# Performance work log

Hardware: AMD Instinct MI355X
Metric: run time of the kernel (lower is better)

Reference implementation:

```python
import jax, jax.numpy as jnp
import numpy as np

B, T, H, W, C = 2, 16, 56, 56, 128
K_T, K = 5, 7
HIDDEN = 4 * C  # expansion_ratio = 4


def kernel_to_freq_3d(kernel, t, h, w):
    # kernel: (C, k_t, k_h, k_w) -> (C, t, h, w) complex freq, centered circular placement
    c, k_t, k_h, k_w = kernel.shape
    t_idx = (jnp.arange(k_t) - k_t // 2) % t
    h_idx = (jnp.arange(k_h) - k_h // 2) % h
    w_idx = (jnp.arange(k_w) - k_w // 2) % w
    tt, th, tw = jnp.meshgrid(t_idx, h_idx, w_idx, indexing='ij')
    padded = jnp.zeros((c, t, h, w), kernel.dtype).at[:, tt, th, tw].set(kernel)
    return jnp.fft.fftn(padded, axes=(1, 2, 3))


def setup_inputs() -> dict:
    key = jax.random.key(0)
    ks = jax.random.split(key, 16)
    n = lambda k, shape, s=0.02: (jax.random.normal(k, shape, jnp.float32) * s)
    return {
        'x': jax.random.normal(ks[0], (B, T, H, W, C), jnp.float32),
        'Wg': n(ks[1], (C, C)), 'bg': jnp.zeros((C,), jnp.float32),
        'Wh': n(ks[2], (C, C)), 'bh': jnp.zeros((C,), jnp.float32),
        'gate_kernel': n(ks[3], (C, K_T, K, K), 0.05),
        'hidden_kernel': n(ks[4], (C, K_T, K, K), 0.05),
        'Wo': n(ks[5], (C, C)), 'bo': jnp.zeros((C,), jnp.float32),
        'ln_scale': jnp.ones((C,), jnp.float32), 'ln_bias': jnp.zeros((C,), jnp.float32),
        'W1': n(ks[6], (C, HIDDEN)), 'b1': jnp.zeros((HIDDEN,), jnp.float32),
        'W2': n(ks[7], (HIDDEN, C)), 'b2': jnp.zeros((C,), jnp.float32),
        'gamma': jnp.full((C,), 1e-6, jnp.float32),
    }


def reference(x, Wg, bg, Wh, bh, gate_kernel, hidden_kernel, Wo, bo,
              ln_scale, ln_bias, W1, b1, W2, b2, gamma):
    b, t, h, w, c = x.shape
    residual = x
    # --- GatedConvSSM3D ---
    gate_proj = x @ Wg + bg
    hidden_proj = x @ Wh + bh
    gk_f = kernel_to_freq_3d(gate_kernel, t, h, w).transpose(1, 2, 3, 0)   # (T,H,W,C)
    hk_f = kernel_to_freq_3d(hidden_kernel, t, h, w).transpose(1, 2, 3, 0)
    gate_spatial = jnp.fft.ifftn(jnp.fft.fftn(gate_proj, axes=(1, 2, 3)) * gk_f[None], axes=(1, 2, 3)).real
    hidden_spatial = jnp.fft.ifftn(jnp.fft.fftn(hidden_proj, axes=(1, 2, 3)) * hk_f[None], axes=(1, 2, 3)).real
    log_forget = -jax.nn.softplus(gate_spatial)          # log(1 - z)
    log_values = -jax.nn.softplus(-gate_spatial) + jnp.log(hidden_spatial ** 2 + 1e-6)  # log z + log h~

    def op(left, right):
        la, lb = left
        ra, rb = right
        return (la + ra, jnp.logaddexp(ra + lb, rb))

    # Heinsen scan along temporal axis (axis=1 of (B,T,H,W,C))
    _, log_h = jax.lax.associative_scan(op, (log_forget, log_values), axis=1)
    ssm_out = jnp.exp(log_h) @ Wo + bo
    # --- LayerNorm3D ---
    mean = jnp.mean(ssm_out, axis=-1, keepdims=True)
    var = jnp.var(ssm_out, axis=-1, keepdims=True)
    xn = (ssm_out - mean) / jnp.sqrt(var + 1e-6) * ln_scale + ln_bias
    # --- MLP + LayerScale + residual ---
    y = jax.nn.gelu(xn @ W1 + b1) @ W2 + b2
    return y * gamma + residual
```

## Files before the change

kernel.cpp:

```cpp
#include <hip/hip_runtime.h>
#include <hip/hip_bf16.h>
#include <hip/hip_fp16.h>
#include <cstdint>
#include <cstddef>

typedef unsigned short u16;
typedef __attribute__((ext_vector_type(8))) short bf16x8;
typedef __attribute__((ext_vector_type(4))) float f32x4;

#define MFMA16(a,b,c) __builtin_amdgcn_mfma_f32_16x16x32_bf16((a),(b),(c),0,0,0)


static __device__ __forceinline__ float b2f(u16 u){ return __uint_as_float(((unsigned)u)<<16); }
static __device__ __forceinline__ u16 f2b(float f){
  unsigned u = __float_as_uint(f);
  return (u16)((u + 0x7fffu + ((u>>16)&1u)) >> 16);
}
static __device__ __forceinline__ u16 f2h(float f){ return __half_as_ushort(__float2half(f)); }
static __device__ __forceinline__ __half2 u2h(unsigned u){ union{unsigned u;__half2 h;}c; c.u=u; return c.h; }

static __device__ __forceinline__ void gld_lds16(const void* g, void* l){
  __builtin_amdgcn_global_load_lds(
      (const __attribute__((address_space(1))) void*)g,
      (__attribute__((address_space(3))) void*)l, 16, 0, 0);
}

static __device__ __forceinline__ bool input_is_f32(const void* xp){
  const u16* u = (const u16*)xp;
  int cnt = 0;
#pragma unroll
  for (int i = 0; i < 64; ++i){
    unsigned e = (u[2*i] >> 7) & 0xFF;
    cnt += (e >= 100 && e <= 140) ? 1 : 0;
  }
  return cnt < 32;
}

static __device__ __forceinline__ u16 ldb(const void* p, int i, bool f32){
  return f32 ? f2b(((const float*)p)[i]) : ((const u16*)p)[i];
}
static __device__ __forceinline__ float ldf(const void* p, int i, bool f32){
  return f32 ? ((const float*)p)[i] : b2f(((const u16*)p)[i]);
}

__global__ __launch_bounds__(256) void k0_prep(
    const void* __restrict__ x,
    const void* __restrict__ Wg, const void* __restrict__ Wh, const void* __restrict__ Wo,
    const void* __restrict__ W1, const void* __restrict__ W2,
    const void* __restrict__ gk, const void* __restrict__ hk,
    const void* __restrict__ bg, const void* __restrict__ bh, const void* __restrict__ bo,
    const void* __restrict__ lns, const void* __restrict__ lnb,
    const void* __restrict__ b1, const void* __restrict__ b2, const void* __restrict__ gm,
    u16* __restrict__ XB,
    u16* __restrict__ WgT, u16* __restrict__ WhT, u16* __restrict__ WoT,
    u16* __restrict__ W1T, u16* __restrict__ W2T,
    unsigned* __restrict__ KWG, unsigned* __restrict__ KWH, u16* __restrict__ PRM)
{
  const bool f32 = input_is_f32(x);
  int tid = blockIdx.x*blockDim.x + threadIdx.x;
  int np  = gridDim.x*blockDim.x;

  if (f32){
    const float* xf = (const float*)x;
    for (int p = tid; p < 6422528; p += np){
      unsigned v = (unsigned)f2b(xf[2*p]) | ((unsigned)f2b(xf[2*p+1]) << 16);
      ((unsigned*)XB)[p] = v;
    }
  } else {
    const unsigned* xu = (const unsigned*)x;
    for (int p = tid; p < 6422528; p += np) ((unsigned*)XB)[p] = xu[p];
  }

  for (int p = tid; p < 16384; p += np){
    int n = p>>7, k = p&127;
    WgT[p] = ldb(Wg, k*128+n, f32);
    WhT[p] = ldb(Wh, k*128+n, f32);
    WoT[p] = ldb(Wo, k*128+n, f32);
  }
  for (int p = tid; p < 65536; p += np){
    int n = p>>7, k = p&127;
    W1T[p] = ldb(W1, k*512+n, f32);
  }
  for (int p = tid; p < 65536; p += np){
    int n = p>>9, k = p&511;
    W2T[p] = ldb(W2, k*128+n, f32);
  }
  for (int p = tid; p < 50176; p += np){
    int tap = p&7, c = (p>>3)&127, jk = p>>10;
    unsigned vg = 0, vh = 0;
    if (tap < 5){
      int s = (c*5+tap)*49 + jk;
      unsigned g16 = f2h(ldf(gk, s, f32)), h16 = f2h(ldf(hk, s, f32));
      vg = g16 | (g16<<16); vh = h16 | (h16<<16);
    }
    KWG[p] = vg; KWH[p] = vh;
  }
  for (int p = tid; p < 1408; p += np){
    const void* src; int off;
    if      (p < 128)  { src = bg;  off = p; }
    else if (p < 256)  { src = bh;  off = p-128; }
    else if (p < 384)  { src = bo;  off = p-256; }
    else if (p < 512)  { src = lns; off = p-384; }
    else if (p < 640)  { src = lnb; off = p-512; }
    else if (p < 1152) { src = b1;  off = p-640; }
    else if (p < 1280) { src = b2;  off = p-1152; }
    else               { src = gm;  off = p-1280; }
    PRM[p] = ldb(src, off, f32);
  }
}

__global__ __launch_bounds__(256) void k1_dualgemm(
    const u16* __restrict__ XB, const u16* __restrict__ WgT, const u16* __restrict__ WhT,
    const u16* __restrict__ PRM,
    u16* __restrict__ GP, u16* __restrict__ HP)
{
  int bid = blockIdx.x;
  int b = bid / 784; int hw = (bid % 784)*4 + (threadIdx.x >> 6);
  int lane = threadIdx.x & 63;
  int lrow = lane & 15, q = lane >> 4;

  bf16x8 a[4];
  const u16* xr = XB + ((size_t)(b*16 + lrow)*3136 + hw)*128 + q*8;
#pragma unroll
  for (int kt = 0; kt < 4; ++kt) a[kt] = *(const bf16x8*)(xr + kt*32);

#pragma unroll
  for (int mat = 0; mat < 2; ++mat){
    const u16* WT  = mat ? WhT : WgT;
    const u16* bia = PRM + (mat ? 128 : 0);
    u16* out       = mat ? HP  : GP;
#pragma unroll
    for (int nt = 0; nt < 8; ++nt){
      f32x4 acc = {0.f,0.f,0.f,0.f};
      const u16* wr = WT + (nt*16 + lrow)*128 + q*8;
#pragma unroll
      for (int kt = 0; kt < 4; ++kt){
        bf16x8 bfr = *(const bf16x8*)(wr + kt*32);
        acc = MFMA16(a[kt], bfr, acc);
      }
      int c = nt*16 + lrow;
      float bv = b2f(bia[c]);
      size_t base = (((size_t)(b*32 + (c>>2))*3136 + hw)*4 + (c&3))*16 + q*4;
      ushort4 pk;
      pk.x = f2h(acc[0] + bv); pk.y = f2h(acc[1] + bv);
      pk.z = f2h(acc[2] + bv); pk.w = f2h(acc[3] + bv);
      *(ushort4*)(out + base) = pk;
    }
  }
}

__global__ __launch_bounds__(256, 5) void k2_conv_scan(
    const u16* __restrict__ GP, const u16* __restrict__ HP,
    const unsigned* __restrict__ KWG, const unsigned* __restrict__ KWH,
    u16* __restrict__ ELH)
{
  __shared__ __align__(16) unsigned su[6272];
  __shared__ __align__(16) unsigned ku[1568];

  int bid = blockIdx.x;
  int b = bid / 1568; int rr = bid - b*1568;
  int cg = rr / 49; int s = rr % 49;
  int th = s / 7, tw = s % 7;
  int tid = threadIdx.x;
  int h0g = th*8, w0g = tw*8;
  size_t tb = (size_t)(b*32 + cg)*200704;

  int cl = tid & 3, w0 = (tid>>2)&7, h0 = tid>>5;
  int wv = tid >> 6, lane = tid & 63;

  unsigned soff[4]; bool sval[4];
#pragma unroll
  for (int ss = 0; ss < 4; ++ss){
    int idx = wv*64 + ss*256 + lane;
    sval[ss] = (idx < 784);
    int pos = idx >> 2, pcl = idx & 3;
    int hh = pos / 14, ww = pos - hh*14;
    int hg = h0g + hh - 3; if (hg < 0) hg += 56; else if (hg >= 56) hg -= 56;
    int wg = w0g + ww - 3; if (wg < 0) wg += 56; else if (wg >= 56) wg -= 56;
    soff[ss] = (unsigned)(((hg*56 + wg)*4 + pcl)*32);
  }
  const char* gpb = (const char*)(GP + tb);
  const char* hpb = (const char*)(HP + tb);

  auto wload = [&](const unsigned* KW){
    for (int p = tid; p < 1568; p += 256){
      int tap = p & 7, c2 = (p>>3)&3, jk = p>>5;
      ku[p] = KW[(jk*128 + cg*4 + c2)*8 + tap];
    }
  };
  auto stagepass = [&](const char* Pb){
#pragma unroll
    for (int half = 0; half < 2; ++half){
#pragma unroll
      for (int ss = 0; ss < 4; ++ss){
        if (sval[ss])
          gld_lds16(Pb + soff[ss] + half*16,
                    (char*)su + half*12544 + (wv*64 + ss*256)*16);
      }
    }
  };
  auto convpass = [&](__half2* A){
#pragma unroll
    for (int p = 0; p < 8; ++p) A[p] = u2h(0u);
    for (int j = 0; j < 7; ++j){
      int hh = h0 + 6 - j;
      int cb0 = ((hh*14 + w0)*4 + cl)*4;
      int wb0 = (j*28 + cl)*8;
#pragma unroll
      for (int k = 0; k < 7; ++k){
        const unsigned* sp = &su[cb0 + (6-k)*16];
        uint4 da = *(const uint4*)sp;
        uint4 db = *(const uint4*)(sp + 3136);
        unsigned P[8] = {da.x,da.y,da.z,da.w,db.x,db.y,db.z,db.w};
        unsigned M[8];
#pragma unroll
        for (int p = 0; p < 8; ++p) M[p] = (P[p]>>16) | (P[(p+1)&7]<<16);
        const unsigned* kp = &ku[wb0 + k*32];
        uint4 w4 = *(const uint4*)kp;
        unsigned w5 = kp[4];
#pragma unroll
        for (int p = 0; p < 8; ++p){
          A[p] = __hfma2(u2h(w4.x), u2h(P[(p+1)&7]), A[p]);
          A[p] = __hfma2(u2h(w4.y), u2h(M[p]),       A[p]);
          A[p] = __hfma2(u2h(w4.z), u2h(P[p]),       A[p]);
          A[p] = __hfma2(u2h(w4.w), u2h(M[(p+7)&7]), A[p]);
          A[p] = __hfma2(u2h(w5),   u2h(P[(p+7)&7]), A[p]);
        }
      }
    }
  };

  __half2 Ag[8], Ah[8];
  wload(KWG);
  stagepass(gpb);
  __syncthreads();
  convpass(Ag);
  __syncthreads();
  wload(KWH);
  stagepass(hpb);
  __syncthreads();
  convpass(Ah);

  float xg[16], xh[16];
#pragma unroll
  for (int p = 0; p < 8; ++p){
    float2 g2 = __half22float2(Ag[p]); xg[2*p] = g2.x; xg[2*p+1] = g2.y;
    float2 h2 = __half22float2(Ah[p]); xh[2*p] = h2.x; xh[2*p+1] = h2.y;
  }

  size_t ob = tb + ((size_t)(h0g + h0)*56 + (w0g + w0))*4 + cl;
  float lh = 0.f;
#pragma unroll
  for (int t = 0; t < 16; ++t){
    float g  = xg[t];
    float spg = fmaxf(g, 0.f) + __logf(1.f + __expf(-fabsf(g)));
    float lf  = -spg;
    float hv  = xh[t];
    float lv  = (g - spg) + __logf(hv*hv + 1e-6f);
    if (t == 0) lh = lv;
    else {
      float a_ = lf + lh;
      float mx = fmaxf(a_, lv);
      lh = mx + __logf(1.f + __expf(-fabsf(a_ - lv)));
    }
    ELH[ob + (size_t)t*12544] = f2b(__expf(lh));
  }
}

__global__ __launch_bounds__(256, 2) void k34_gemm_ln_mlp(
    const u16* __restrict__ ELH, const u16* __restrict__ WoT,
    const u16* __restrict__ W1T, const u16* __restrict__ W2T,
    const u16* __restrict__ PRM,
    const void* __restrict__ xraw, void* __restrict__ outv)
{
  __shared__ __align__(16) u16 smem[37376];
  u16* sW0 = smem;
  u16* sW1 = smem + 16384;
  u16* sXp = smem;
  u16* sH  = smem + 32768;

  int bid = blockIdx.x;
  int b = bid / 392; int rem = bid - b*392;
  int t2 = rem / 49; int s2 = rem - t2*49;
  int hw0 = s2 * 64;
  int tid = threadIdx.x;
  int wv = tid >> 6, lane = tid & 63;
  int lrow = lane & 15, q = lane >> 4;
  const bool f32io = input_is_f32(xraw);

  {
    int hw = hw0 + wv*16 + lrow;
    size_t tbA = ((size_t)(b*512) + t2)*3136;
    size_t tbB = tbA + (size_t)8*3136;
    union Cvt { uint4 u; bf16x8 v; };
    bf16x8 eA[4], eB[4];
#pragma unroll
    for (int kt = 0; kt < 4; ++kt){
      int cg0 = kt*8 + q*2;
      size_t eoA = (tbA + (size_t)cg0*50176 + hw)*4;
      size_t eoB = (tbB + (size_t)cg0*50176 + hw)*4;
      uint2 lo = *(const uint2*)(ELH + eoA);
      uint2 hi = *(const uint2*)(ELH + eoA + (size_t)50176*4);
      Cvt c1; c1.u = make_uint4(lo.x, lo.y, hi.x, hi.y); eA[kt] = c1.v;
      uint2 lo2 = *(const uint2*)(ELH + eoB);
      uint2 hi2 = *(const uint2*)(ELH + eoB + (size_t)50176*4);
      Cvt c2; c2.u = make_uint4(lo2.x, lo2.y, hi2.x, hi2.y); eB[kt] = c2.v;
    }

    float vA[8][4], vB[8][4];
#pragma unroll
    for (int nt = 0; nt < 8; ++nt){
      f32x4 aacc = {0.f,0.f,0.f,0.f}, bacc = {0.f,0.f,0.f,0.f};
      const u16* wr = WoT + (nt*16 + lrow)*128 + q*8;
#pragma unroll
      for (int kt = 0; kt < 4; ++kt){
        bf16x8 bfr = *(const bf16x8*)(wr + kt*32);
        aacc = MFMA16(eA[kt], bfr, aacc);
        bacc = MFMA16(eB[kt], bfr, bacc);
      }
      float bv = b2f(PRM[256 + nt*16 + lrow]);
#pragma unroll
      for (int i = 0; i < 4; ++i){ vA[nt][i] = aacc[i] + bv; vB[nt][i] = bacc[i] + bv; }
    }

#pragma unroll
    for (int i = 0; i < 4; ++i){
      float smA=0.f, sqA=0.f, smB=0.f, sqB=0.f;
#pragma unroll
      for (int nt = 0; nt < 8; ++nt){
        float a_ = vA[nt][i]; smA += a_; sqA = fmaf(a_, a_, sqA);
        float b_ = vB[nt][i]; smB += b_; sqB = fmaf(b_, b_, sqB);
      }
#pragma unroll
      for (int m = 1; m < 16; m <<= 1){
        smA += __shfl_xor(smA, m, 64); sqA += __shfl_xor(sqA, m, 64);
        smB += __shfl_xor(smB, m, 64); sqB += __shfl_xor(sqB, m, 64);
      }
      float mA = smA*(1.f/128.f), rA = rsqrtf(sqA*(1.f/128.f) - mA*mA + 1e-6f);
      float mB = smB*(1.f/128.f), rB = rsqrtf(sqB*(1.f/128.f) - mB*mB + 1e-6f);
      int r = wv*16 + q*4 + i;
#pragma unroll
      for (int nt = 0; nt < 8; ++nt){
        int c = nt*16 + lrow;
        float ls = b2f(PRM[384 + c]), lb = b2f(PRM[512 + c]);
        sXp[r*136 + c]        = f2b((vA[nt][i] - mA)*rA*ls + lb);
        sXp[8704 + r*136 + c] = f2b((vB[nt][i] - mB)*rB*ls + lb);
      }
    }
  }

  bf16x8 aA[4], aB[4];
#pragma unroll
  for (int kt = 0; kt < 4; ++kt){
    aA[kt] = *(const bf16x8*)&sXp[(wv*16 + lrow)*136 + kt*32 + q*8];
    aB[kt] = *(const bf16x8*)&sXp[8704 + (wv*16 + lrow)*136 + kt*32 + q*8];
  }
  __syncthreads();

  const u16* wsrc[8];
#pragma unroll
  for (int r = 0; r < 8; ++r){
    int c = r*4 + wv;
    if (c < 16){
      int j = c >> 2, kt = c & 3;
      wsrc[r] = W1T + (size_t)(j*16 + lrow)*128 + kt*32 + q*8;
    } else {
      int c2 = c - 16; int jo = c2 >> 1, kt2 = c2 & 1;
      wsrc[r] = W2T + (size_t)(jo*16 + lrow)*512 + kt2*32 + q*8;
    }
  }
  auto stage = [&](u16* buf, int nt){
#pragma unroll
    for (int r = 0; r < 8; ++r){
      int c = r*4 + wv;
      const u16* src = wsrc[r] + (c < 16 ? (size_t)nt*8192 : (size_t)nt*64);
      gld_lds16(src, buf + c*512);
    }
  };

  f32x4 accA[8], accB[8];
#pragma unroll
  for (int jo = 0; jo < 8; ++jo){ accA[jo] = (f32x4){0.f,0.f,0.f,0.f}; accB[jo] = (f32x4){0.f,0.f,0.f,0.f}; }
  u16* sHw = sH + wv*1152;

  stage(sW0, 0);
  asm volatile("s_waitcnt vmcnt(0)" ::: "memory");
  __builtin_amdgcn_s_barrier();

  auto mlpstep = [&](int nt, u16* wcur, u16* wnxt, bool do_stage){
    if (do_stage) stage(wnxt, nt+1);
#pragma unroll
    for (int js = 0; js < 4; ++js){
      f32x4 hc = {0.f,0.f,0.f,0.f};
#pragma unroll
      for (int kt = 0; kt < 4; ++kt)
        hc = MFMA16(aA[kt], *(const bf16x8*)&wcur[(js*4 + kt)*512 + lane*8], hc);
      float bv = b2f(PRM[640 + nt*64 + js*16 + lrow]);
#pragma unroll
      for (int i = 0; i < 4; ++i){
        float v = hc[i] + bv;
        float u = 0.79788456080286535588f*(v + 0.044715f*v*v*v);
        float su_ = __expf(-2.f*u);
        float gl = v * __builtin_amdgcn_rcpf(1.f + su_);
        sHw[(q*4 + i)*72 + js*16 + lrow] = (u16)(__float_as_uint(gl) >> 16);
      }
    }
#pragma unroll
    for (int kt2 = 0; kt2 < 2; ++kt2){
      bf16x8 af = *(const bf16x8*)&sHw[lrow*72 + kt2*32 + q*8];
#pragma unroll
      for (int jo = 0; jo < 8; ++jo)
        accA[jo] = MFMA16(af, *(const bf16x8*)&wcur[(16 + jo*2 + kt2)*512 + lane*8], accA[jo]);
    }
#pragma unroll
    for (int js = 0; js < 4; ++js){
      f32x4 hc = {0.f,0.f,0.f,0.f};
#pragma unroll
      for (int kt = 0; kt < 4; ++kt)
        hc = MFMA16(aB[kt], *(const bf16x8*)&wcur[(js*4 + kt)*512 + lane*8], hc);
      float bv = b2f(PRM[640 + nt*64 + js*16 + lrow]);
#pragma unroll
      for (int i = 0; i < 4; ++i){
        float v = hc[i] + bv;
        float u = 0.79788456080286535588f*(v + 0.044715f*v*v*v);
        float su_ = __expf(-2.f*u);
        float gl = v * __builtin_amdgcn_rcpf(1.f + su_);
        sHw[(q*4 + i)*72 + js*16 + lrow] = (u16)(__float_as_uint(gl) >> 16);
      }
    }
#pragma unroll
    for (int kt2 = 0; kt2 < 2; ++kt2){
      bf16x8 af = *(const bf16x8*)&sHw[lrow*72 + kt2*32 + q*8];
#pragma unroll
      for (int jo = 0; jo < 8; ++jo)
        accB[jo] = MFMA16(af, *(const bf16x8*)&wcur[(16 + jo*2 + kt2)*512 + lane*8], accB[jo]);
    }
    asm volatile("s_waitcnt vmcnt(0)" ::: "memory");
    __builtin_amdgcn_s_barrier();
  };

  for (int nt2 = 0; nt2 < 4; ++nt2){
    mlpstep(2*nt2,     sW0, sW1, true);
    mlpstep(2*nt2 + 1, sW1, sW0, nt2 < 3);
  }

  size_t rowA0 = ((size_t)(b*16 + t2))*3136 + hw0 + wv*16 + q*4;
  size_t rowB0 = rowA0 + (size_t)8*3136;
#pragma unroll
  for (int jo = 0; jo < 8; ++jo){
    int c = jo*16 + lrow;
    float bv  = b2f(PRM[1152 + c]);
    float gmv = b2f(PRM[1280 + c]);
#pragma unroll
    for (int i = 0; i < 4; ++i){
      size_t rA = rowA0 + i, rB = rowB0 + i;
      float yA = accA[jo][i] + bv, yB = accB[jo][i] + bv;
      if (f32io){
        float resA = ((const float*)xraw)[rA*128 + c];
        float resB = ((const float*)xraw)[rB*128 + c];
        ((float*)outv)[rA*128 + c] = yA*gmv + resA;
        ((float*)outv)[rB*128 + c] = yB*gmv + resB;
      } else {
        float resA = b2f(((const u16*)xraw)[rA*128 + c]);
        float resB = b2f(((const u16*)xraw)[rB*128 + c]);
        ((u16*)outv)[rA*128 + c] = f2b(yA*gmv + resA);
        ((u16*)outv)[rB*128 + c] = f2b(yB*gmv + resB);
      }
    }
  }
}

extern "C" void kernel_launch(void* const* d_in, const int* in_sizes, int n_in,
                              void* d_out, int out_size, void* d_ws, size_t ws_size,
                              hipStream_t stream)
{
  const void* x   = d_in[0];
  const void* Wg  = d_in[1];
  const void* bg  = d_in[2];
  const void* Wh  = d_in[3];
  const void* bh  = d_in[4];
  const void* gk  = d_in[5];
  const void* hk  = d_in[6];
  const void* Wo  = d_in[7];
  const void* bo  = d_in[8];
  const void* lns = d_in[9];
  const void* lnb = d_in[10];
  const void* W1  = d_in[11];
  const void* b1  = d_in[12];
  const void* W2  = d_in[13];
  const void* b2  = d_in[14];
  const void* gm  = d_in[15];

  char* ws = (char*)d_ws;
  u16* GP  = (u16*)(ws + 0);
  u16* HP  = (u16*)(ws + 25690112);
  u16* ELH = (u16*)(ws + 51380224);
  u16* XB  = (u16*)(ws + 77070336);
  u16* WgT = (u16*)(ws + 102760448);
  u16* WhT = WgT + 16384;
  u16* WoT = WhT + 16384;
  u16* W1T = WoT + 16384;
  u16* W2T = W1T + 65536;
  unsigned* KWG = (unsigned*)(W2T + 65536);
  unsigned* KWH = KWG + 50176;
  u16* PRM = (u16*)(KWH + 50176);

  k0_prep        <<<dim3(512),  dim3(256), 0, stream>>>(x, Wg, Wh, Wo, W1, W2, gk, hk,
                                                        bg, bh, bo, lns, lnb, b1, b2, gm,
                                                        XB, WgT, WhT, WoT, W1T, W2T, KWG, KWH, PRM);
  k1_dualgemm    <<<dim3(1568), dim3(256), 0, stream>>>(XB, WgT, WhT, PRM, GP, HP);
  k2_conv_scan   <<<dim3(3136), dim3(256), 0, stream>>>(GP, HP, KWG, KWH, ELH);
  k34_gemm_ln_mlp<<<dim3(784),  dim3(256), 0, stream>>>(ELH, WoT, W1T, W2T, PRM, x, (void*)d_out);
}
```

Before: 453.6 us.

## Map one channel per wavefront so conv weights load as uniform scalar reads

Changes the thread mapping in the depthwise conv+scan kernel so each wavefront owns a single channel. Conv weights can then be read through a wave-uniform pointer (readfirstlane) straight from global memory instead of being staged in LDS. The weight pack drops its padding taps, and the staged input tile uses an XOR swizzle on the channel slot to avoid LDS bank conflicts under the new mapping. Launch bounds rise to 6 blocks per CU, using the LDS freed by removing the weight buffer. The 35 preloaded weights per row add register pressure.

Measured after the change: 446.0 us. No clear change (-1.7%).

```diff
diff --git a/kernel.cpp b/kernel.cpp
--- a/kernel.cpp
+++ b/kernel.cpp
@@ -85,15 +85,14 @@
     int n = p>>9, k = p&511;
     W2T[p] = ldb(W2, k*128+n, f32);
   }
-  for (int p = tid; p < 50176; p += np){
-    int tap = p&7, c = (p>>3)&127, jk = p>>10;
-    unsigned vg = 0, vh = 0;
-    if (tap < 5){
-      int s = (c*5+tap)*49 + jk;
-      unsigned g16 = f2h(ldf(gk, s, f32)), h16 = f2h(ldf(hk, s, f32));
-      vg = g16 | (g16<<16); vh = h16 | (h16<<16);
-    }
-    KWG[p] = vg; KWH[p] = vh;
+  for (int p = tid; p < 31360; p += np){
+    int c = p / 245; int r = p - c*245;
+    int j = r / 35;  int r2 = r - j*35;
+    int k = r2 / 5;  int tap = r2 - k*5;
+    int s = (c*5+tap)*49 + (j*7+k);
+    unsigned g16 = f2h(ldf(gk, s, f32)), h16 = f2h(ldf(hk, s, f32));
+    KWG[p] = g16 | (g16<<16);
+    KWH[p] = h16 | (h16<<16);
   }
   for (int p = tid; p < 1408; p += np){
     const void* src; int off;
@@ -149,13 +148,12 @@
   }
 }
 
-__global__ __launch_bounds__(256, 5) void k2_conv_scan(
+__global__ __launch_bounds__(256, 6) void k2_conv_scan(
     const u16* __restrict__ GP, const u16* __restrict__ HP,
     const unsigned* __restrict__ KWG, const unsigned* __restrict__ KWH,
     u16* __restrict__ ELH)
 {
   __shared__ __align__(16) unsigned su[6272];
-  __shared__ __align__(16) unsigned ku[1568];
 
   int bid = blockIdx.x;
   int b = bid / 1568; int rr = bid - b*1568;
@@ -165,16 +163,22 @@
   int h0g = th*8, w0g = tw*8;
   size_t tb = (size_t)(b*32 + cg)*200704;
 
-  int cl = tid & 3, w0 = (tid>>2)&7, h0 = tid>>5;
   int wv = tid >> 6, lane = tid & 63;
+  int cl = wv;
+  int w0 = lane & 7, h0 = lane >> 3;
+
+  int cu = __builtin_amdgcn_readfirstlane(cg*4 + wv);
+  const unsigned* kwg = KWG + (size_t)cu*245;
+  const unsigned* kwh = KWH + (size_t)cu*245;
 
   unsigned soff[4]; bool sval[4];
 #pragma unroll
   for (int ss = 0; ss < 4; ++ss){
     int idx = wv*64 + ss*256 + lane;
     sval[ss] = (idx < 784);
-    int pos = idx >> 2, pcl = idx & 3;
+    int pos = idx >> 2, d = idx & 3;
     int hh = pos / 14, ww = pos - hh*14;
+    int pcl = d ^ (hh & 3);
     int hg = h0g + hh - 3; if (hg < 0) hg += 56; else if (hg >= 56) hg -= 56;
     int wg = w0g + ww - 3; if (wg < 0) wg += 56; else if (wg >= 56) wg -= 56;
     soff[ss] = (unsigned)(((hg*56 + wg)*4 + pcl)*32);
@@ -182,12 +186,6 @@
   const char* gpb = (const char*)(GP + tb);
   const char* hpb = (const char*)(HP + tb);
 
-  auto wload = [&](const unsigned* KW){
-    for (int p = tid; p < 1568; p += 256){
-      int tap = p & 7, c2 = (p>>3)&3, jk = p>>5;
-      ku[p] = KW[(jk*128 + cg*4 + c2)*8 + tap];
-    }
-  };
   auto stagepass = [&](const char* Pb){
 #pragma unroll
     for (int half = 0; half < 2; ++half){
@@ -199,13 +197,15 @@
       }
     }
   };
-  auto convpass = [&](__half2* A){
+  auto convpass = [&](__half2* A, const unsigned* kw){
 #pragma unroll
     for (int p = 0; p < 8; ++p) A[p] = u2h(0u);
     for (int j = 0; j < 7; ++j){
       int hh = h0 + 6 - j;
-      int cb0 = ((hh*14 + w0)*4 + cl)*4;
-      int wb0 = (j*28 + cl)*8;
+      int cb0 = (hh*14 + w0)*16 + ((cl ^ (hh & 3)) << 2);
+      unsigned wj[35];
+#pragma unroll
+      for (int i = 0; i < 35; ++i) wj[i] = kw[j*35 + i];
 #pragma unroll
       for (int k = 0; k < 7; ++k){
         const unsigned* sp = &su[cb0 + (6-k)*16];
@@ -215,31 +215,26 @@
         unsigned M[8];
 #pragma unroll
         for (int p = 0; p < 8; ++p) M[p] = (P[p]>>16) | (P[(p+1)&7]<<16);
-        const unsigned* kp = &ku[wb0 + k*32];
-        uint4 w4 = *(const uint4*)kp;
-        unsigned w5 = kp[4];
 #pragma unroll
         for (int p = 0; p < 8; ++p){
-          A[p] = __hfma2(u2h(w4.x), u2h(P[(p+1)&7]), A[p]);
-          A[p] = __hfma2(u2h(w4.y), u2h(M[p]),       A[p]);
-          A[p] = __hfma2(u2h(w4.z), u2h(P[p]),       A[p]);
-          A[p] = __hfma2(u2h(w4.w), u2h(M[(p+7)&7]), A[p]);
-          A[p] = __hfma2(u2h(w5),   u2h(P[(p+7)&7]), A[p]);
+          A[p] = __hfma2(u2h(wj[k*5+0]), u2h(P[(p+1)&7]), A[p]);
+          A[p] = __hfma2(u2h(wj[k*5+1]), u2h(M[p]),       A[p]);
+          A[p] = __hfma2(u2h(wj[k*5+2]), u2h(P[p]),       A[p]);
+          A[p] = __hfma2(u2h(wj[k*5+3]), u2h(M[(p+7)&7]), A[p]);
+          A[p] = __hfma2(u2h(wj[k*5+4]), u2h(P[(p+7)&7]), A[p]);
         }
       }
     }
   };
 
   __half2 Ag[8], Ah[8];
-  wload(KWG);
   stagepass(gpb);
   __syncthreads();
-  convpass(Ag);
+  convpass(Ag, kwg);
   __syncthreads();
-  wload(KWH);
   stagepass(hpb);
   __syncthreads();
-  convpass(Ah);
+  convpass(Ah, kwh);
 
   float xg[16], xh[16];
 #pragma unroll
```
